# Performance work log

Hardware: AMD Instinct MI355X
Metric: run time of the kernel (lower is better)

Reference implementation:

```python
import jax, jax.numpy as jnp
import numpy as np


def _ln(x, w, b):
    m = x.mean(-1, keepdims=True)
    v = ((x - m) ** 2).mean(-1, keepdims=True)
    return (x - m) / jnp.sqrt(v + 1e-5) * w + b


def setup_inputs() -> dict:
    key = jax.random.key(0)
    ks = jax.random.split(key, 8)
    N, C, H, W = 2, 64, 128, 128
    heads, ksz = 2, 7
    C4 = 4 * C
    p = lambda k, shape: jax.random.normal(k, shape, dtype=jnp.float32) * 0.02
    return {
        "x": jax.random.normal(ks[0], (N, C, H, W), dtype=jnp.float32),
        "qkv_w": p(ks[1], (3 * C, C)),
        "qkv_b": jnp.zeros((3 * C,), jnp.float32),
        "proj_w": p(ks[2], (C, C)),
        "proj_b": jnp.zeros((C,), jnp.float32),
        "rpb": p(ks[3], (heads, 2 * ksz - 1, 2 * ksz - 1)),
        "ln1_w": jnp.ones((C,), jnp.float32),
        "ln1_b": jnp.zeros((C,), jnp.float32),
        "ln2_w": jnp.ones((C,), jnp.float32),
        "ln2_b": jnp.zeros((C,), jnp.float32),
        "fc1_w": p(ks[4], (C4, C)),
        "fc1_b": jnp.zeros((C4,), jnp.float32),
        "fc2_w": p(ks[5], (C, C4)),
        "fc2_b": jnp.zeros((C,), jnp.float32),
    }


def reference(x, qkv_w, qkv_b, proj_w, proj_b, rpb, ln1_w, ln1_b, ln2_w, ln2_b,
              fc1_w, fc1_b, fc2_w, fc2_b):
    N, C, H, W = x.shape
    heads = rpb.shape[0]
    ksz = (rpb.shape[1] + 1) // 2  # kernel size from (2k-1) bias table
    dh = C // heads

    xt = x.transpose(0, 2, 3, 1).reshape(N, H * W, C)  # n (h w) c
    shortcut = xt
    xn = _ln(xt, ln1_w, ln1_b).reshape(N, H, W, C)

    # qkv projection -> (3, N, heads, H, W, dh)
    qkv = (xn @ qkv_w.T + qkv_b).reshape(N, H, W, 3, heads, dh)
    qkv = qkv.transpose(3, 0, 4, 1, 2, 5)
    q = qkv[0] * (dh ** -0.5)
    k = qkv[1]
    v = qkv[2]

    # NATTEN neighborhood: window start clamped so every query sees k x k keys
    sh = jnp.clip(jnp.arange(H) - ksz // 2, 0, H - ksz)
    sw = jnp.clip(jnp.arange(W) - ksz // 2, 0, W - ksz)
    rows = sh[:, None] + jnp.arange(ksz)  # (H, k) key row indices
    cols = sw[:, None] + jnp.arange(ksz)  # (W, k) key col indices

    # relative position bias index: (query - key) + (k-1) in [0, 2k-2]
    rel_h = jnp.arange(H)[:, None] - rows + (ksz - 1)  # (H, k)
    rel_w = jnp.arange(W)[:, None] - cols + (ksz - 1)  # (W, k)
    bias = rpb[:, rel_h][:, :, :, rel_w]               # (heads, H, k, W, k)
    bias = bias.transpose(0, 1, 3, 2, 4)               # (heads, H, W, k, k)

    ri = rows[:, None, :, None]  # (H,1,k,1)
    ci = cols[None, :, None, :]  # (1,W,1,k)
    kwin = k[:, :, ri, ci, :]    # (N, heads, H, W, k, k, dh)
    vwin = v[:, :, ri, ci, :]

    scores = jnp.einsum('nzhwd,nzhwijd->nzhwij', q, kwin) + bias[None]
    attn = jax.nn.softmax(scores.reshape(N, heads, H, W, ksz * ksz), axis=-1)
    out = jnp.einsum('nzhwe,nzhwed->nzhwd', attn,
                     vwin.reshape(N, heads, H, W, ksz * ksz, dh))
    out = out.transpose(0, 2, 3, 1, 4).reshape(N, H, W, C) @ proj_w.T + proj_b

    x2 = shortcut + out.reshape(N, H * W, C)
    y = _ln(x2, ln2_w, ln2_b)
    y = jax.nn.gelu(y @ fc1_w.T + fc1_b, approximate=False) @ fc2_w.T + fc2_b
    x3 = x2 + y
    return x3.reshape(N, H, W, C).transpose(0, 3, 1, 2)
```

## Files before the change

### kernel.cpp

```cpp
#include <hip/hip_runtime.h>
#include <math.h>

#define TQ   32768
#define HWSZ 16384
#define CC   64
#define HH   128
#define WW   128
#define C3   192
#define C4   256
#define KS   7

typedef _Float16 half2v __attribute__((ext_vector_type(2)));
typedef _Float16 half4v __attribute__((ext_vector_type(4)));
typedef _Float16 half8v __attribute__((ext_vector_type(8)));
typedef float    f32x4  __attribute__((ext_vector_type(4)));

#define MFMA16(a, b, c) __builtin_amdgcn_mfma_f32_16x16x32_f16((a), (b), (c), 0, 0, 0)

__global__ __launch_bounds__(256) void k_qkvln(const float* __restrict__ x,
        const float* __restrict__ lnw, const float* __restrict__ lnb,
        const float* __restrict__ qw, const float* __restrict__ qb,
        _Float16* __restrict__ qkv16) {
    __shared__ union {
        struct { __align__(16) _Float16 A[128 * 72]; __align__(16) _Float16 B[192 * 72]; } st;
        __align__(16) _Float16 outb[128 * 200];
    } u;
    __shared__ float ps1[256], ps2[256], m_s[128], r_s[128];
    __shared__ float w_s[64], b_s[64], bias_s[192];
    int tid = threadIdx.x;
    int t0 = blockIdx.x * 128;
    if (tid < 64) { w_s[tid] = lnw[tid]; b_s[tid] = lnb[tid]; }
    if (tid < 192) bias_s[tid] = qb[tid];
    int tok = tid & 127, cq = tid >> 7;
    int t = t0 + tok;
    int n = t >> 14, hw = t & (HWSZ - 1);
    const float* xr = x + ((size_t)n << 20) + hw;
    float v[32];
    float s = 0.f, s2 = 0.f;
#pragma unroll
    for (int e = 0; e < 32; ++e) {
        float f = xr[(cq * 32 + e) * HWSZ];
        v[e] = f; s += f; s2 += f * f;
    }
    ps1[tid] = s; ps2[tid] = s2;
    for (int i = tid; i < 3072; i += 256) {
        int jj = i >> 4, seg = i & 15;
        float4 v4 = *(const float4*)&qw[(size_t)jj * 64 + seg * 4];
        half4v h4 = { (_Float16)v4.x, (_Float16)v4.y, (_Float16)v4.z, (_Float16)v4.w };
        *(half4v*)&u.st.B[jj * 72 + seg * 4] = h4;
    }
    __syncthreads();
    if (tid < 128) {
        float ss = ps1[tid] + ps1[tid + 128];
        float qq = ps2[tid] + ps2[tid + 128];
        float m = ss * (1.f / 64.f);
        float var = qq * (1.f / 64.f) - m * m;
        m_s[tid] = m; r_s[tid] = rsqrtf(var + 1e-5f);
    }
    __syncthreads();
    {
        float m = m_s[tok], r = r_s[tok];
#pragma unroll
        for (int u8 = 0; u8 < 4; ++u8) {
            half8v o;
#pragma unroll
            for (int e = 0; e < 8; ++e) {
                int c = cq * 32 + u8 * 8 + e;
                o[e] = (_Float16)((v[u8 * 8 + e] - m) * r * w_s[c] + b_s[c]);
            }
            *(half8v*)&u.st.A[tok * 72 + cq * 32 + u8 * 8] = o;
        }
    }
    __syncthreads();
    int lane = tid & 63, wv = tid >> 6;
    int quad = lane >> 4, l16 = lane & 15;
    int mt0 = (wv & 1) * 64, nt0 = (wv >> 1) * 96;
    f32x4 acc[4][6];
#pragma unroll
    for (int mf = 0; mf < 4; ++mf)
#pragma unroll
        for (int nf = 0; nf < 6; ++nf) acc[mf][nf] = (f32x4){0.f, 0.f, 0.f, 0.f};
#pragma unroll
    for (int ks = 0; ks < 64; ks += 32) {
        half8v a[4], bfr[6];
#pragma unroll
        for (int mf = 0; mf < 4; ++mf)
            a[mf] = *(const half8v*)&u.st.A[(mt0 + mf * 16 + l16) * 72 + ks + quad * 8];
#pragma unroll
        for (int nf = 0; nf < 6; ++nf)
            bfr[nf] = *(const half8v*)&u.st.B[(nt0 + nf * 16 + l16) * 72 + ks + quad * 8];
#pragma unroll
        for (int mf = 0; mf < 4; ++mf)
#pragma unroll
            for (int nf = 0; nf < 6; ++nf) acc[mf][nf] = MFMA16(a[mf], bfr[nf], acc[mf][nf]);
    }
    __syncthreads();
    const float qscale = 0.17677669529663687f;
#pragma unroll
    for (int mf = 0; mf < 4; ++mf)
#pragma unroll
        for (int nf = 0; nf < 6; ++nf) {
            int j = nt0 + nf * 16 + l16;
            float bias = bias_s[j];
            float sc = (j < 64) ? qscale : 1.f;
#pragma unroll
            for (int r = 0; r < 4; ++r) {
                int tl = mt0 + mf * 16 + quad * 4 + r;
                u.outb[tl * 200 + j] = (_Float16)((acc[mf][nf][r] + bias) * sc);
            }
        }
    __syncthreads();
    for (int i = tid; i < 4096; i += 256) {
        int tk = i >> 5, rem = i & 31;
        if (rem < 24)
            *(half8v*)&qkv16[(size_t)(t0 + tk) * C3 + rem * 8] =
                *(const half8v*)&u.outb[tk * 200 + rem * 8];
    }
}

#define KV_STRIDE 136
#define QS_STRIDE 80
#define SS_STRIDE 50

__global__ __launch_bounds__(256) void k_attn(const _Float16* __restrict__ qkv16,
        const float* __restrict__ rpb, _Float16* __restrict__ out) {
    __shared__ __align__(16) _Float16 kv_s[196 * KV_STRIDE];
    __shared__ __align__(16) _Float16 q_s[64 * QS_STRIDE];
    __shared__ __align__(16) _Float16 s_s[128 * SS_STRIDE];
    __shared__ float rpb_s[338];

    int tid = threadIdx.x;
    int bx = blockIdx.x;
    int n  = bx >> 8;
    int th = (bx >> 4) & 15, tw = bx & 15;
    int h0 = th * 8, w0 = tw * 8;
    int wr0 = min(max(h0 - 3, 0), HH - 14);
    int ww0 = min(max(w0 - 3, 0), WW - 14);
    int tbase = n << 14;

    for (int i = tid; i < 338; i += 256) rpb_s[i] = rpb[i];
    for (int i = tid; i < 196 * 16; i += 256) {
        int tok = i >> 4, u = i & 15;
        int wi = tok / 14, wj = tok - wi * 14;
        *(half8v*)&kv_s[tok * KV_STRIDE + u * 8] = *(const half8v*)&qkv16[
            (size_t)(tbase + (wr0 + wi) * WW + ww0 + wj) * C3 + 64 + u * 8];
    }
    for (int i = tid; i < 64 * 8; i += 256) {
        int q = i >> 3, u = i & 7;
        int qg = tbase + (h0 + (q >> 3)) * WW + (w0 + (q & 7));
        *(half8v*)&q_s[q * QS_STRIDE + u * 8] = *(const half8v*)&qkv16[(size_t)qg * C3 + u * 8];
    }
    __syncthreads();

    int half_ = tid & 1, z = (tid >> 1) & 1, q = tid >> 2;
    int qy = q >> 3, qx = q & 7;
    int h = h0 + qy, wc = w0 + qx;
    int sh = min(max(h - 3, 0), HH - KS);
    int sw = min(max(wc - 3, 0), WW - KS);
    int oh = sh - wr0, ow = sw - ww0;
    int dhp = h - sh + 6, dwp = wc - sw + 6;
    {
        const half8v* qp = (const half8v*)&q_s[q * QS_STRIDE + z * 32];
        half8v q0 = qp[0], q1 = qp[1], q2 = qp[2], q3 = qp[3];
        int i7 = 0, j7 = half_;
        for (int nb = half_; nb < 49; nb += 2) {
            int tok = (oh + i7) * 14 + (ow + j7);
            const half8v* kp = (const half8v*)&kv_s[tok * KV_STRIDE + z * 32];
            half2v acc2 = { (_Float16)0.f, (_Float16)0.f };
            half8v k0 = kp[0], k1 = kp[1], k2 = kp[2], k3 = kp[3];
            acc2 += (half2v){k0.s0, k0.s1} * (half2v){q0.s0, q0.s1};
            acc2 += (half2v){k0.s2, k0.s3} * (half2v){q0.s2, q0.s3};
            acc2 += (half2v){k0.s4, k0.s5} * (half2v){q0.s4, q0.s5};
            acc2 += (half2v){k0.s6, k0.s7} * (half2v){q0.s6, q0.s7};
            acc2 += (half2v){k1.s0, k1.s1} * (half2v){q1.s0, q1.s1};
            acc2 += (half2v){k1.s2, k1.s3} * (half2v){q1.s2, q1.s3};
            acc2 += (half2v){k1.s4, k1.s5} * (half2v){q1.s4, q1.s5};
            acc2 += (half2v){k1.s6, k1.s7} * (half2v){q1.s6, q1.s7};
            acc2 += (half2v){k2.s0, k2.s1} * (half2v){q2.s0, q2.s1};
            acc2 += (half2v){k2.s2, k2.s3} * (half2v){q2.s2, q2.s3};
            acc2 += (half2v){k2.s4, k2.s5} * (half2v){q2.s4, q2.s5};
            acc2 += (half2v){k2.s6, k2.s7} * (half2v){q2.s6, q2.s7};
            acc2 += (half2v){k3.s0, k3.s1} * (half2v){q3.s0, q3.s1};
            acc2 += (half2v){k3.s2, k3.s3} * (half2v){q3.s2, q3.s3};
            acc2 += (half2v){k3.s4, k3.s5} * (half2v){q3.s4, q3.s5};
            acc2 += (half2v){k3.s6, k3.s7} * (half2v){q3.s6, q3.s7};
            float s = (float)acc2.x + (float)acc2.y
                    + rpb_s[(z * 13 + (dhp - i7)) * 13 + (dwp - j7)];
            s_s[(q * 2 + z) * SS_STRIDE + nb] = (_Float16)s;
            j7 += 2;
            if (j7 >= 7) { j7 -= 7; ++i7; }
        }
    }
    __syncthreads();

    if (tid < 128) {
        _Float16* sp = &s_s[tid * SS_STRIDE];
        float mx = -1e30f;
        for (int i = 0; i < 49; ++i) mx = fmaxf(mx, (float)sp[i]);
        float sum = 0.f;
        for (int i = 0; i < 49; ++i) {
            float e = __expf((float)sp[i] - mx);
            sum += e;
            sp[i] = (_Float16)e;
        }
        float inv = 1.f / sum;
        for (int i = 0; i < 49; ++i) sp[i] = (_Float16)((float)sp[i] * inv);
    }
    __syncthreads();

    {
        int c16 = half_;
        const _Float16* pp = &s_s[(q * 2 + z) * SS_STRIDE];
        half2v acc[8];
#pragma unroll
        for (int j = 0; j < 8; ++j) acc[j] = (half2v){ (_Float16)0.f, (_Float16)0.f };
        int i7 = 0, j7 = 0;
        for (int nb = 0; nb < 49; ++nb) {
            int tok = (oh + i7) * 14 + (ow + j7);
            _Float16 p = pp[nb];
            half2v p2 = { p, p };
            const half8v* vp = (const half8v*)&kv_s[tok * KV_STRIDE + 64 + z * 32 + c16 * 16];
            half8v v0 = vp[0], v1 = vp[1];
            acc[0] += (half2v){v0.s0, v0.s1} * p2;
            acc[1] += (half2v){v0.s2, v0.s3} * p2;
            acc[2] += (half2v){v0.s4, v0.s5} * p2;
            acc[3] += (half2v){v0.s6, v0.s7} * p2;
            acc[4] += (half2v){v1.s0, v1.s1} * p2;
            acc[5] += (half2v){v1.s2, v1.s3} * p2;
            acc[6] += (half2v){v1.s4, v1.s5} * p2;
            acc[7] += (half2v){v1.s6, v1.s7} * p2;
            ++j7;
            if (j7 == 7) { j7 = 0; ++i7; }
        }
        int qg = tbase + h * WW + wc;
        _Float16* op = out + (size_t)qg * CC + z * 32 + c16 * 16;
        half8v o0 = {acc[0].x, acc[0].y, acc[1].x, acc[1].y, acc[2].x, acc[2].y, acc[3].x, acc[3].y};
        half8v o1 = {acc[4].x, acc[4].y, acc[5].x, acc[5].y, acc[6].x, acc[6].y, acc[7].x, acc[7].y};
        *(half8v*)op = o0;
        *(half8v*)(op + 8) = o1;
    }
}

__global__ __launch_bounds__(256) void k_projln(const _Float16* __restrict__ ain,
        const float* __restrict__ pw, const float* __restrict__ pb,
        const float* __restrict__ x,
        const float* __restrict__ ln2w, const float* __restrict__ ln2b,
        _Float16* __restrict__ x2_16, _Float16* __restrict__ xn2_16) {
    __shared__ union {
        struct { __align__(16) _Float16 A[128 * 72]; __align__(16) _Float16 B[64 * 72]; } st;
        float x2t[128 * 67];
    } u;
    __shared__ float ps1[256], ps2[256], m_s[128], r_s[128];
    __shared__ float w_s[64], b_s[64], pbias[64];
    int tid = threadIdx.x;
    int t0 = blockIdx.x * 128;
    int n = t0 >> 14, hw0 = t0 & (HWSZ - 1);
    if (tid < 64) { w_s[tid] = ln2w[tid]; b_s[tid] = ln2b[tid]; pbias[tid] = pb[tid]; }
    for (int i = tid; i < 1024; i += 256) {
        int tok = i >> 3, u8 = i & 7;
        *(half8v*)&u.st.A[tok * 72 + u8 * 8] = *(const half8v*)&ain[(size_t)(t0 + tok) * 64 + u8 * 8];
    }
    for (int i = tid; i < 1024; i += 256) {
        int jj = i >> 4, seg = i & 15;
        float4 v4 = *(const float4*)&pw[(size_t)jj * 64 + seg * 4];
        half4v h4 = { (_Float16)v4.x, (_Float16)v4.y, (_Float16)v4.z, (_Float16)v4.w };
        *(half4v*)&u.st.B[jj * 72 + seg * 4] = h4;
    }
    __syncthreads();
    int lane = tid & 63, wv = tid >> 6;
    int quad = lane >> 4, l16 = lane & 15;
    int mt0 = wv * 32;
    f32x4 acc[2][4];
#pragma unroll
    for (int mf = 0; mf < 2; ++mf)
#pragma unroll
        for (int nf = 0; nf < 4; ++nf) acc[mf][nf] = (f32x4){0.f, 0.f, 0.f, 0.f};
#pragma unroll
    for (int ks = 0; ks < 64; ks += 32) {
        half8v a[2], bfr[4];
#pragma unroll
        for (int mf = 0; mf < 2; ++mf)
            a[mf] = *(const half8v*)&u.st.A[(mt0 + mf * 16 + l16) * 72 + ks + quad * 8];
#pragma unroll
        for (int nf = 0; nf < 4; ++nf)
            bfr[nf] = *(const half8v*)&u.st.B[(nf * 16 + l16) * 72 + ks + quad * 8];
#pragma unroll
        for (int mf = 0; mf < 2; ++mf)
#pragma unroll
            for (int nf = 0; nf < 4; ++nf) acc[mf][nf] = MFMA16(a[mf], bfr[nf], acc[mf][nf]);
    }
    __syncthreads();
#pragma unroll
    for (int mf = 0; mf < 2; ++mf)
#pragma unroll
        for (int nf = 0; nf < 4; ++nf) {
            int j = nf * 16 + l16;
            float bias = pbias[j];
            int hwl = hw0 + mt0 + mf * 16 + quad * 4;
            float4 rx = *(const float4*)&x[((size_t)(n * CC + j) << 14) + hwl];
#pragma unroll
            for (int r = 0; r < 4; ++r) {
                int tl = mt0 + mf * 16 + quad * 4 + r;
                u.x2t[tl * 67 + j] = acc[mf][nf][r] + bias + ((const float*)&rx)[r];
            }
        }
    __syncthreads();
    int tok = tid & 127, cq = tid >> 7;
    {
        float s = 0.f, s2 = 0.f;
#pragma unroll
        for (int e = 0; e < 32; ++e) {
            float f = u.x2t[tok * 67 + cq * 32 + e];
            s += f; s2 += f * f;
        }
        ps1[tid] = s; ps2[tid] = s2;
    }
    __syncthreads();
    if (tid < 128) {
        float ss = ps1[tid] + ps1[tid + 128];
        float qq = ps2[tid] + ps2[tid + 128];
        float m = ss * (1.f / 64.f);
        float var = qq * (1.f / 64.f) - m * m;
        m_s[tid] = m; r_s[tid] = rsqrtf(var + 1e-5f);
    }
    __syncthreads();
    {
        float m = m_s[tok], r = r_s[tok];
#pragma unroll
        for (int u8 = 0; u8 < 4; ++u8) {
            half8v hv, nv;
#pragma unroll
            for (int e = 0; e < 8; ++e) {
                int c = cq * 32 + u8 * 8 + e;
                float f = u.x2t[tok * 67 + c];
                hv[e] = (_Float16)f;
                nv[e] = (_Float16)((f - m) * r * w_s[c] + b_s[c]);
            }
            size_t base = (size_t)(t0 + tok) * 64 + cq * 32 + u8 * 8;
            *(half8v*)&x2_16[base] = hv;
            *(half8v*)&xn2_16[base] = nv;
        }
    }
}

__global__ __launch_bounds__(256) void k_mlp(const _Float16* __restrict__ xn2,
        const _Float16* __restrict__ x2_16,
        const float* __restrict__ f1w, const float* __restrict__ f1b,
        const float* __restrict__ f2w, const float* __restrict__ f2b,
        float* __restrict__ out) {
    __shared__ __align__(16) _Float16 H_s[64 * 264];
    __shared__ union {
        struct { __align__(16) _Float16 A[64 * 72]; __align__(16) _Float16 B[128 * 72]; } st;
        float tr[64 * 68];
    } u;
    __shared__ float f1b_s[256], f2b_s[64];
    int tid = threadIdx.x;
    int t0 = blockIdx.x * 64;
    int lane = tid & 63, wv = tid >> 6;
    int quad = lane >> 4, l16 = lane & 15;
    f1b_s[tid] = f1b[tid];
    if (tid < 64) f2b_s[tid] = f2b[tid];
    for (int i = tid; i < 512; i += 256) {
        int tok = i >> 3, u8 = i & 7;
        *(half8v*)&u.st.A[tok * 72 + u8 * 8] = *(const half8v*)&xn2[(size_t)(t0 + tok) * 64 + u8 * 8];
    }
    for (int jh = 0; jh < 2; ++jh) {
        if (jh) __syncthreads();
        for (int i = tid; i < 2048; i += 256) {
            int jj = i >> 4, seg = i & 15;
            float4 v4 = *(const float4*)&f1w[(size_t)(jh * 128 + jj) * 64 + seg * 4];
            half4v h4 = { (_Float16)v4.x, (_Float16)v4.y, (_Float16)v4.z, (_Float16)v4.w };
            *(half4v*)&u.st.B[jj * 72 + seg * 4] = h4;
        }
        __syncthreads();
        int mt0 = (wv & 1) * 32, nt0 = (wv >> 1) * 64;
        f32x4 acc[2][4];
#pragma unroll
        for (int mf = 0; mf < 2; ++mf)
#pragma unroll
            for (int nf = 0; nf < 4; ++nf) acc[mf][nf] = (f32x4){0.f, 0.f, 0.f, 0.f};
#pragma unroll
        for (int ks = 0; ks < 64; ks += 32) {
            half8v a[2], bfr[4];
#pragma unroll
            for (int mf = 0; mf < 2; ++mf)
                a[mf] = *(const half8v*)&u.st.A[(mt0 + mf * 16 + l16) * 72 + ks + quad * 8];
#pragma unroll
            for (int nf = 0; nf < 4; ++nf)
                bfr[nf] = *(const half8v*)&u.st.B[(nt0 + nf * 16 + l16) * 72 + ks + quad * 8];
#pragma unroll
            for (int mf = 0; mf < 2; ++mf)
#pragma unroll
                for (int nf = 0; nf < 4; ++nf) acc[mf][nf] = MFMA16(a[mf], bfr[nf], acc[mf][nf]);
        }
#pragma unroll
        for (int mf = 0; mf < 2; ++mf)
#pragma unroll
            for (int nf = 0; nf < 4; ++nf) {
                int jl = nt0 + nf * 16 + l16;
                float bias = f1b_s[jh * 128 + jl];
#pragma unroll
                for (int r = 0; r < 4; ++r) {
                    int tl = mt0 + mf * 16 + quad * 4 + r;
                    float vv = acc[mf][nf][r] + bias;
                    float g = 0.5f * vv * (1.f + erff(vv * 0.70710678118654752f));
                    H_s[tl * 264 + jh * 128 + jl] = (_Float16)g;
                }
            }
    }
    __syncthreads();
    int mt0 = wv * 16;
    f32x4 acc2[4];
#pragma unroll
    for (int nf = 0; nf < 4; ++nf) acc2[nf] = (f32x4){0.f, 0.f, 0.f, 0.f};
    for (int kp = 0; kp < 4; ++kp) {
        if (kp) __syncthreads();
        for (int i = tid; i < 1024; i += 256) {
            int jj = i >> 4, seg = i & 15;
            float4 v4 = *(const float4*)&f2w[(size_t)jj * C4 + kp * 64 + seg * 4];
            half4v h4 = { (_Float16)v4.x, (_Float16)v4.y, (_Float16)v4.z, (_Float16)v4.w };
            *(half4v*)&u.st.B[jj * 72 + seg * 4] = h4;
        }
        __syncthreads();
#pragma unroll
        for (int ks = 0; ks < 64; ks += 32) {
            half8v a = *(const half8v*)&H_s[(mt0 + l16) * 264 + kp * 64 + ks + quad * 8];
            half8v bfr[4];
#pragma unroll
            for (int nf = 0; nf < 4; ++nf)
                bfr[nf] = *(const half8v*)&u.st.B[(nf * 16 + l16) * 72 + ks + quad * 8];
#pragma unroll
            for (int nf = 0; nf < 4; ++nf) acc2[nf] = MFMA16(a, bfr[nf], acc2[nf]);
        }
    }
    __syncthreads();
#pragma unroll
    for (int nf = 0; nf < 4; ++nf) {
        int j = nf * 16 + l16;
        float bias = f2b_s[j];
#pragma unroll
        for (int r = 0; r < 4; ++r) {
            int tl = mt0 + quad * 4 + r;
            float v = acc2[nf][r] + bias + (float)x2_16[(size_t)(t0 + tl) * 64 + j];
            u.tr[j * 68 + tl] = v;
        }
    }
    __syncthreads();
    int n = t0 >> 14, hw0 = t0 & (HWSZ - 1);
    for (int i = tid; i < 1024; i += 256) {
        int j = i >> 4, seg = i & 15;
        float4 v = *(const float4*)&u.tr[j * 68 + seg * 4];
        *(float4*)&out[((size_t)(n * CC + j) << 14) + hw0 + seg * 4] = v;
    }
}

extern "C" void kernel_launch(void* const* d_in, const int* in_sizes, int n_in,
                              void* d_out, int out_size, void* d_ws, size_t ws_size,
                              hipStream_t stream) {
    const float* x      = (const float*)d_in[0];
    const float* qkv_w  = (const float*)d_in[1];
    const float* qkv_b  = (const float*)d_in[2];
    const float* proj_w = (const float*)d_in[3];
    const float* proj_b = (const float*)d_in[4];
    const float* rpb    = (const float*)d_in[5];
    const float* ln1_w  = (const float*)d_in[6];
    const float* ln1_b  = (const float*)d_in[7];
    const float* ln2_w  = (const float*)d_in[8];
    const float* ln2_b  = (const float*)d_in[9];
    const float* fc1_w  = (const float*)d_in[10];
    const float* fc1_b  = (const float*)d_in[11];
    const float* fc2_w  = (const float*)d_in[12];
    const float* fc2_b  = (const float*)d_in[13];
    float* out = (float*)d_out;
    char* ws = (char*)d_ws;

    _Float16* qkv16  = (_Float16*)(ws);
    _Float16* attn16 = (_Float16*)(ws + 12582912);
    _Float16* x2_16  = (_Float16*)(ws + 16777216);
    _Float16* xn2_16 = (_Float16*)(ws + 20971520);

    k_qkvln <<<256, 256, 0, stream>>>(x, ln1_w, ln1_b, qkv_w, qkv_b, qkv16);
    k_attn  <<<512, 256, 0, stream>>>(qkv16, rpb, attn16);
    k_projln<<<256, 256, 0, stream>>>(attn16, proj_w, proj_b, x, ln2_w, ln2_b, x2_16, xn2_16);
    k_mlp   <<<512, 256, 0, stream>>>(xn2_16, x2_16, fc1_w, fc1_b, fc2_w, fc2_b, out);
}
```

Before: 142.9 us.

## Fuse attention with projection and LN2; pre-convert weights to fp16 once

Merges the attention kernel with the output projection, residual add and second layernorm, so the attention output stays in shared memory instead of going through a global fp16 buffer and a separate launch. The projection and MLP weights are converted to fp16 once, inside the first kernel, and later kernels load them with wide fp16 reads instead of converting fp32 per block. The fused kernel uses about 77KB of aliased shared memory, which may lower occupancy. The fused block also handles only 64 tokens for the projection GEMM.

Measured after the change: 132.6 us. 7.2% less time.

```diff
diff --git a/kernel.cpp b/kernel.cpp
--- a/kernel.cpp
+++ b/kernel.cpp
@@ -20,7 +20,10 @@
 __global__ __launch_bounds__(256) void k_qkvln(const float* __restrict__ x,
         const float* __restrict__ lnw, const float* __restrict__ lnb,
         const float* __restrict__ qw, const float* __restrict__ qb,
-        _Float16* __restrict__ qkv16) {
+        const float* __restrict__ pw, const float* __restrict__ f1w,
+        const float* __restrict__ f2w,
+        _Float16* __restrict__ qkv16, _Float16* __restrict__ pw16,
+        _Float16* __restrict__ f1w16, _Float16* __restrict__ f2w16) {
     __shared__ union {
         struct { __align__(16) _Float16 A[128 * 72]; __align__(16) _Float16 B[192 * 72]; } st;
         __align__(16) _Float16 outb[128 * 200];
@@ -49,6 +52,12 @@
         half4v h4 = { (_Float16)v4.x, (_Float16)v4.y, (_Float16)v4.z, (_Float16)v4.w };
         *(half4v*)&u.st.B[jj * 72 + seg * 4] = h4;
     }
+    {
+        int g = blockIdx.x * 256 + tid;
+        if (g < 4096) pw16[g] = (_Float16)pw[g];
+        else if (g < 20480) f1w16[g - 4096] = (_Float16)f1w[g - 4096];
+        else if (g < 36864) f2w16[g - 20480] = (_Float16)f2w[g - 20480];
+    }
     __syncthreads();
     if (tid < 128) {
         float ss = ps1[tid] + ps1[tid + 128];
@@ -118,16 +127,25 @@
     }
 }
 
-#define KV_STRIDE 136
-#define QS_STRIDE 80
-#define SS_STRIDE 50
-
-__global__ __launch_bounds__(256) void k_attn(const _Float16* __restrict__ qkv16,
-        const float* __restrict__ rpb, _Float16* __restrict__ out) {
-    __shared__ __align__(16) _Float16 kv_s[196 * KV_STRIDE];
-    __shared__ __align__(16) _Float16 q_s[64 * QS_STRIDE];
-    __shared__ __align__(16) _Float16 s_s[128 * SS_STRIDE];
-    __shared__ float rpb_s[338];
+__global__ __launch_bounds__(256) void k_attnproj(const _Float16* __restrict__ qkv16,
+        const float* __restrict__ rpb,
+        const _Float16* __restrict__ pw16, const float* __restrict__ pb,
+        const float* __restrict__ x,
+        const float* __restrict__ ln2w, const float* __restrict__ ln2b,
+        _Float16* __restrict__ x2_16, _Float16* __restrict__ xn2_16) {
+    __shared__ __align__(16) char smem[77704];
+    _Float16* kv_s  = (_Float16*)smem;
+    _Float16* q_s   = (_Float16*)(smem + 53312);
+    _Float16* s_s   = (_Float16*)(smem + 63552);
+    float*    rpb_s = (float*)(smem + 76352);
+    float* x2t  = (float*)smem;
+    float* ps1  = (float*)(smem + 20480);
+    float* ps2  = (float*)(smem + 21504);
+    float* m_s  = (float*)(smem + 22528);
+    float* r_s  = (float*)(smem + 22784);
+    float* w_s  = (float*)(smem + 23040);
+    float* b_s  = (float*)(smem + 23296);
+    float* pb_s = (float*)(smem + 23552);
 
     int tid = threadIdx.x;
     int bx = blockIdx.x;
@@ -137,22 +155,24 @@
     int wr0 = min(max(h0 - 3, 0), HH - 14);
     int ww0 = min(max(w0 - 3, 0), WW - 14);
     int tbase = n << 14;
+    int lane = tid & 63, wvi = tid >> 6;
+    int quad = lane >> 4, l16 = lane & 15;
 
     for (int i = tid; i < 338; i += 256) rpb_s[i] = rpb[i];
     for (int i = tid; i < 196 * 16; i += 256) {
         int tok = i >> 4, u = i & 15;
         int wi = tok / 14, wj = tok - wi * 14;
-        *(half8v*)&kv_s[tok * KV_STRIDE + u * 8] = *(const half8v*)&qkv16[
+        *(half8v*)&kv_s[tok * 136 + u * 8] = *(const half8v*)&qkv16[
             (size_t)(tbase + (wr0 + wi) * WW + ww0 + wj) * C3 + 64 + u * 8];
     }
     for (int i = tid; i < 64 * 8; i += 256) {
         int q = i >> 3, u = i & 7;
         int qg = tbase + (h0 + (q >> 3)) * WW + (w0 + (q & 7));
-        *(half8v*)&q_s[q * QS_STRIDE + u * 8] = *(const half8v*)&qkv16[(size_t)qg * C3 + u * 8];
-    }
-    __syncthreads();
-
-    int half_ = tid & 1, z = (tid >> 1) & 1, q = tid >> 2;
+        *(half8v*)&q_s[q * 80 + u * 8] = *(const half8v*)&qkv16[(size_t)qg * C3 + u * 8];
+    }
+    __syncthreads();
+
+    int c16 = tid & 1, z = (tid >> 1) & 1, q = tid >> 2;
     int qy = q >> 3, qx = q & 7;
     int h = h0 + qy, wc = w0 + qx;
     int sh = min(max(h - 3, 0), HH - KS);
@@ -160,12 +180,12 @@
     int oh = sh - wr0, ow = sw - ww0;
     int dhp = h - sh + 6, dwp = wc - sw + 6;
     {
-        const half8v* qp = (const half8v*)&q_s[q * QS_STRIDE + z * 32];
+        const half8v* qp = (const half8v*)&q_s[q * 80 + z * 32];
         half8v q0 = qp[0], q1 = qp[1], q2 = qp[2], q3 = qp[3];
-        int i7 = 0, j7 = half_;
-        for (int nb = half_; nb < 49; nb += 2) {
+        int i7 = 0, j7 = c16;
+        for (int nb = c16; nb < 49; nb += 2) {
             int tok = (oh + i7) * 14 + (ow + j7);
-            const half8v* kp = (const half8v*)&kv_s[tok * KV_STRIDE + z * 32];
+            const half8v* kp = (const half8v*)&kv_s[tok * 136 + z * 32];
             half2v acc2 = { (_Float16)0.f, (_Float16)0.f };
             half8v k0 = kp[0], k1 = kp[1], k2 = kp[2], k3 = kp[3];
             acc2 += (half2v){k0.s0, k0.s1} * (half2v){q0.s0, q0.s1};
@@ -186,7 +206,7 @@
             acc2 += (half2v){k3.s6, k3.s7} * (half2v){q3.s6, q3.s7};
             float s = (float)acc2.x + (float)acc2.y
                     + rpb_s[(z * 13 + (dhp - i7)) * 13 + (dwp - j7)];
-            s_s[(q * 2 + z) * SS_STRIDE + nb] = (_Float16)s;
+            s_s[(q * 2 + z) * 50 + nb] = (_Float16)s;
             j7 += 2;
             if (j7 >= 7) { j7 -= 7; ++i7; }
         }
@@ -194,7 +214,7 @@
     __syncthreads();
 
     if (tid < 128) {
-        _Float16* sp = &s_s[tid * SS_STRIDE];
+        _Float16* sp = &s_s[tid * 50];
         float mx = -1e30f;
         for (int i = 0; i < 49; ++i) mx = fmaxf(mx, (float)sp[i]);
         float sum = 0.f;
@@ -209,8 +229,7 @@
     __syncthreads();
 
     {
-        int c16 = half_;
-        const _Float16* pp = &s_s[(q * 2 + z) * SS_STRIDE];
+        const _Float16* pp = &s_s[(q * 2 + z) * 50];
         half2v acc[8];
 #pragma unroll
         for (int j = 0; j < 8; ++j) acc[j] = (half2v){ (_Float16)0.f, (_Float16)0.f };
@@ -219,7 +238,7 @@
             int tok = (oh + i7) * 14 + (ow + j7);
             _Float16 p = pp[nb];
             half2v p2 = { p, p };
-            const half8v* vp = (const half8v*)&kv_s[tok * KV_STRIDE + 64 + z * 32 + c16 * 16];
+            const half8v* vp = (const half8v*)&kv_s[tok * 136 + 64 + z * 32 + c16 * 16];
             half8v v0 = vp[0], v1 = vp[1];
             acc[0] += (half2v){v0.s0, v0.s1} * p2;
             acc[1] += (half2v){v0.s2, v0.s3} * p2;
@@ -232,93 +251,62 @@
             ++j7;
             if (j7 == 7) { j7 = 0; ++i7; }
         }
-        int qg = tbase + h * WW + wc;
-        _Float16* op = out + (size_t)qg * CC + z * 32 + c16 * 16;
+        _Float16* op = q_s + q * 72 + z * 32 + c16 * 16;
         half8v o0 = {acc[0].x, acc[0].y, acc[1].x, acc[1].y, acc[2].x, acc[2].y, acc[3].x, acc[3].y};
         half8v o1 = {acc[4].x, acc[4].y, acc[5].x, acc[5].y, acc[6].x, acc[6].y, acc[7].x, acc[7].y};
         *(half8v*)op = o0;
         *(half8v*)(op + 8) = o1;
     }
-}
-
-__global__ __launch_bounds__(256) void k_projln(const _Float16* __restrict__ ain,
-        const float* __restrict__ pw, const float* __restrict__ pb,
-        const float* __restrict__ x,
-        const float* __restrict__ ln2w, const float* __restrict__ ln2b,
-        _Float16* __restrict__ x2_16, _Float16* __restrict__ xn2_16) {
-    __shared__ union {
-        struct { __align__(16) _Float16 A[128 * 72]; __align__(16) _Float16 B[64 * 72]; } st;
-        float x2t[128 * 67];
-    } u;
-    __shared__ float ps1[256], ps2[256], m_s[128], r_s[128];
-    __shared__ float w_s[64], b_s[64], pbias[64];
-    int tid = threadIdx.x;
-    int t0 = blockIdx.x * 128;
-    int n = t0 >> 14, hw0 = t0 & (HWSZ - 1);
-    if (tid < 64) { w_s[tid] = ln2w[tid]; b_s[tid] = ln2b[tid]; pbias[tid] = pb[tid]; }
-    for (int i = tid; i < 1024; i += 256) {
-        int tok = i >> 3, u8 = i & 7;
-        *(half8v*)&u.st.A[tok * 72 + u8 * 8] = *(const half8v*)&ain[(size_t)(t0 + tok) * 64 + u8 * 8];
-    }
-    for (int i = tid; i < 1024; i += 256) {
-        int jj = i >> 4, seg = i & 15;
-        float4 v4 = *(const float4*)&pw[(size_t)jj * 64 + seg * 4];
-        half4v h4 = { (_Float16)v4.x, (_Float16)v4.y, (_Float16)v4.z, (_Float16)v4.w };
-        *(half4v*)&u.st.B[jj * 72 + seg * 4] = h4;
-    }
-    __syncthreads();
-    int lane = tid & 63, wv = tid >> 6;
-    int quad = lane >> 4, l16 = lane & 15;
-    int mt0 = wv * 32;
-    f32x4 acc[2][4];
-#pragma unroll
-    for (int mf = 0; mf < 2; ++mf)
-#pragma unroll
-        for (int nf = 0; nf < 4; ++nf) acc[mf][nf] = (f32x4){0.f, 0.f, 0.f, 0.f};
-#pragma unroll
-    for (int ks = 0; ks < 64; ks += 32) {
-        half8v a[2], bfr[4];
-#pragma unroll
-        for (int mf = 0; mf < 2; ++mf)
-            a[mf] = *(const half8v*)&u.st.A[(mt0 + mf * 16 + l16) * 72 + ks + quad * 8];
-#pragma unroll
-        for (int nf = 0; nf < 4; ++nf)
-            bfr[nf] = *(const half8v*)&u.st.B[(nf * 16 + l16) * 72 + ks + quad * 8];
-#pragma unroll
-        for (int mf = 0; mf < 2; ++mf)
-#pragma unroll
-            for (int nf = 0; nf < 4; ++nf) acc[mf][nf] = MFMA16(a[mf], bfr[nf], acc[mf][nf]);
-    }
-    __syncthreads();
-#pragma unroll
-    for (int mf = 0; mf < 2; ++mf)
+    __syncthreads();
+    for (int i = tid; i < 512; i += 256) {
+        int jj = i >> 3, c8 = i & 7;
+        *(half8v*)&s_s[jj * 72 + c8 * 8] = *(const half8v*)&pw16[jj * 64 + c8 * 8];
+    }
+    if (tid < 64) { w_s[tid] = ln2w[tid]; b_s[tid] = ln2b[tid]; pb_s[tid] = pb[tid]; }
+    __syncthreads();
+    {
+        int mt0 = wvi * 16;
+        f32x4 acc2[4];
+#pragma unroll
+        for (int nf = 0; nf < 4; ++nf) acc2[nf] = (f32x4){0.f, 0.f, 0.f, 0.f};
+#pragma unroll
+        for (int ks = 0; ks < 64; ks += 32) {
+            half8v a = *(const half8v*)&q_s[(mt0 + l16) * 72 + ks + quad * 8];
+            half8v bfr[4];
+#pragma unroll
+            for (int nf = 0; nf < 4; ++nf)
+                bfr[nf] = *(const half8v*)&s_s[(nf * 16 + l16) * 72 + ks + quad * 8];
+#pragma unroll
+            for (int nf = 0; nf < 4; ++nf) acc2[nf] = MFMA16(a, bfr[nf], acc2[nf]);
+        }
+        __syncthreads();
+        int tl0 = mt0 + quad * 4;
+        int hwl = (h0 + (tl0 >> 3)) * WW + w0 + (tl0 & 7);
 #pragma unroll
         for (int nf = 0; nf < 4; ++nf) {
             int j = nf * 16 + l16;
-            float bias = pbias[j];
-            int hwl = hw0 + mt0 + mf * 16 + quad * 4;
+            float bias = pb_s[j];
             float4 rx = *(const float4*)&x[((size_t)(n * CC + j) << 14) + hwl];
 #pragma unroll
-            for (int r = 0; r < 4; ++r) {
-                int tl = mt0 + mf * 16 + quad * 4 + r;
-                u.x2t[tl * 67 + j] = acc[mf][nf][r] + bias + ((const float*)&rx)[r];
-            }
-        }
-    __syncthreads();
-    int tok = tid & 127, cq = tid >> 7;
+            for (int r = 0; r < 4; ++r)
+                x2t[(tl0 + r) * 68 + j] = acc2[nf][r] + bias + ((const float*)&rx)[r];
+        }
+    }
+    __syncthreads();
+    int tok = tid & 63, cq = tid >> 6;
     {
         float s = 0.f, s2 = 0.f;
 #pragma unroll
-        for (int e = 0; e < 32; ++e) {
-            float f = u.x2t[tok * 67 + cq * 32 + e];
+        for (int e = 0; e < 16; ++e) {
+            float f = x2t[tok * 68 + cq * 16 + e];
             s += f; s2 += f * f;
         }
         ps1[tid] = s; ps2[tid] = s2;
     }
     __syncthreads();
-    if (tid < 128) {
-        float ss = ps1[tid] + ps1[tid + 128];
-        float qq = ps2[tid] + ps2[tid + 128];
+    if (tid < 64) {
+        float ss = ps1[tid] + ps1[64 + tid] + ps1[128 + tid] + ps1[192 + tid];
+        float qq = ps2[tid] + ps2[64 + tid] + ps2[128 + tid] + ps2[192 + tid];
         float m = ss * (1.f / 64.f);
         float var = qq * (1.f / 64.f) - m * m;
         m_s[tid] = m; r_s[tid] = rsqrtf(var + 1e-5f);
@@ -326,27 +314,32 @@
     __syncthreads();
     {
         float m = m_s[tok], r = r_s[tok];
-#pragma unroll
-        for (int u8 = 0; u8 < 4; ++u8) {
-            half8v hv, nv;
-#pragma unroll
-            for (int e = 0; e < 8; ++e) {
-                int c = cq * 32 + u8 * 8 + e;
-                float f = u.x2t[tok * 67 + c];
-                hv[e] = (_Float16)f;
-                nv[e] = (_Float16)((f - m) * r * w_s[c] + b_s[c]);
-            }
-            size_t base = (size_t)(t0 + tok) * 64 + cq * 32 + u8 * 8;
-            *(half8v*)&x2_16[base] = hv;
-            *(half8v*)&xn2_16[base] = nv;
-        }
+        int qg = tbase + (h0 + (tok >> 3)) * WW + (w0 + (tok & 7));
+        half8v hv0, hv1, nv0, nv1;
+#pragma unroll
+        for (int e = 0; e < 8; ++e) {
+            int c = cq * 16 + e;
+            float f = x2t[tok * 68 + c];
+            hv0[e] = (_Float16)f;
+            nv0[e] = (_Float16)((f - m) * r * w_s[c] + b_s[c]);
+        }
+#pragma unroll
+        for (int e = 0; e < 8; ++e) {
+            int c = cq * 16 + 8 + e;
+            float f = x2t[tok * 68 + c];
+            hv1[e] = (_Float16)f;
+            nv1[e] = (_Float16)((f - m) * r * w_s[c] + b_s[c]);
+        }
+        size_t base = (size_t)qg * 64 + cq * 16;
+        *(half8v*)&x2_16[base] = hv0;  *(half8v*)&x2_16[base + 8] = hv1;
+        *(half8v*)&xn2_16[base] = nv0; *(half8v*)&xn2_16[base + 8] = nv1;
     }
 }
 
 __global__ __launch_bounds__(256) void k_mlp(const _Float16* __restrict__ xn2,
         const _Float16* __restrict__ x2_16,
-        const float* __restrict__ f1w, const float* __restrict__ f1b,
-        const float* __restrict__ f2w, const float* __restrict__ f2b,
+        const _Float16* __restrict__ f1w16, const float* __restrict__ f1b,
+        const _Float16* __restrict__ f2w16, const float* __restrict__ f2b,
         float* __restrict__ out) {
     __shared__ __align__(16) _Float16 H_s[64 * 264];
     __shared__ union {
@@ -366,11 +359,10 @@
     }
     for (int jh = 0; jh < 2; ++jh) {
         if (jh) __syncthreads();
-        for (int i = tid; i < 2048; i += 256) {
-            int jj = i >> 4, seg = i & 15;
-            float4 v4 = *(const float4*)&f1w[(size_t)(jh * 128 + jj) * 64 + seg * 4];
-            half4v h4 = { (_Float16)v4.x, (_Float16)v4.y, (_Float16)v4.z, (_Float16)v4.w };
-            *(half4v*)&u.st.B[jj * 72 + seg * 4] = h4;
+        for (int i = tid; i < 1024; i += 256) {
+            int jj = i >> 3, c8 = i & 7;
+            *(half8v*)&u.st.B[jj * 72 + c8 * 8] =
+                *(const half8v*)&f1w16[(size_t)(jh * 128 + jj) * 64 + c8 * 8];
         }
         __syncthreads();
         int mt0 = (wv & 1) * 32, nt0 = (wv >> 1) * 64;
@@ -415,11 +407,10 @@
     for (int nf = 0; nf < 4; ++nf) acc2[nf] = (f32x4){0.f, 0.f, 0.f, 0.f};
     for (int kp = 0; kp < 4; ++kp) {
         if (kp) __syncthreads();
-        for (int i = tid; i < 1024; i += 256) {
-            int jj = i >> 4, seg = i & 15;
-            float4 v4 = *(const float4*)&f2w[(size_t)jj * C4 + kp * 64 + seg * 4];
-            half4v h4 = { (_Float16)v4.x, (_Float16)v4.y, (_Float16)v4.z, (_Float16)v4.w };
-            *(half4v*)&u.st.B[jj * 72 + seg * 4] = h4;
+        for (int i = tid; i < 512; i += 256) {
+            int jj = i >> 3, c8 = i & 7;
+            *(half8v*)&u.st.B[jj * 72 + c8 * 8] =
+                *(const half8v*)&f2w16[(size_t)jj * C4 + kp * 64 + c8 * 8];
         }
         __syncthreads();
 #pragma unroll
@@ -475,12 +466,16 @@
     char* ws = (char*)d_ws;
 
     _Float16* qkv16  = (_Float16*)(ws);
-    _Float16* attn16 = (_Float16*)(ws + 12582912);
-    _Float16* x2_16  = (_Float16*)(ws + 16777216);
-    _Float16* xn2_16 = (_Float16*)(ws + 20971520);
-
-    k_qkvln <<<256, 256, 0, stream>>>(x, ln1_w, ln1_b, qkv_w, qkv_b, qkv16);
-    k_attn  <<<512, 256, 0, stream>>>(qkv16, rpb, attn16);
-    k_projln<<<256, 256, 0, stream>>>(attn16, proj_w, proj_b, x, ln2_w, ln2_b, x2_16, xn2_16);
-    k_mlp   <<<512, 256, 0, stream>>>(xn2_16, x2_16, fc1_w, fc1_b, fc2_w, fc2_b, out);
+    _Float16* x2_16  = (_Float16*)(ws + 12582912);
+    _Float16* xn2_16 = (_Float16*)(ws + 16777216);
+    _Float16* pw16   = (_Float16*)(ws + 20971520);
+    _Float16* f1w16  = (_Float16*)(ws + 20979712);
+    _Float16* f2w16  = (_Float16*)(ws + 21012480);
+
+    k_qkvln   <<<256, 256, 0, stream>>>(x, ln1_w, ln1_b, qkv_w, qkv_b,
+                                        proj_w, fc1_w, fc2_w,
+                                        qkv16, pw16, f1w16, f2w16);
+    k_attnproj<<<512, 256, 0, stream>>>(qkv16, rpb, pw16, proj_b, x, ln2_w, ln2_b,
+                                        x2_16, xn2_16);
+    k_mlp     <<<512, 256, 0, stream>>>(xn2_16, x2_16, f1w16, fc1_b, f2w16, fc2_b, out);
 }
```
